# Performance work log

Hardware: AMD Instinct MI355X
Metric: run time of the kernel (lower is better)

Reference implementation:

```python
import jax, jax.numpy as jnp
import numpy as np

HID = 2048 * 3  # infl_ratio = 3
EPS = 1e-5
P_DROP = 0.5


def sign_ste(x):
    # straight-through binarization: sign in fwd, identity in bwd
    return x + jax.lax.stop_gradient(jnp.sign(x) - x)


def batchnorm(x, g, b):
    # training-mode BatchNorm1d: batch stats, biased variance
    m = jnp.mean(x, axis=0)
    v = jnp.mean((x - m) ** 2, axis=0)
    return g * (x - m) / jnp.sqrt(v + EPS) + b


def hardtanh(x):
    return jnp.clip(x, -1.0, 1.0)


def dropout(x, u):
    # u ~ U[0,1); keep where u >= p, scale by 1/(1-p)
    return jnp.where(u >= P_DROP, x / (1.0 - P_DROP), 0.0)


def setup_inputs() -> dict:
    key = jax.random.key(0)
    ks = jax.random.split(key, 16)
    B = 512
    d = {}
    d['x'] = jax.random.normal(ks[0], (B, 784), dtype=jnp.float32)
    d['drop_mask_bin'] = jax.random.uniform(ks[1], (B, HID), dtype=jnp.float32)
    d['drop_mask_real'] = jax.random.uniform(ks[2], (B, HID), dtype=jnp.float32)
    s1 = 1.0 / np.sqrt(784)
    sh = 1.0 / np.sqrt(HID)
    d['w1'] = jax.random.uniform(ks[3], (HID, 784), jnp.float32, -s1, s1)
    d['b1'] = jax.random.uniform(ks[4], (HID,), jnp.float32, -s1, s1)
    d['w2'] = jax.random.uniform(ks[5], (HID, HID), jnp.float32, -sh, sh)
    d['b2'] = jax.random.uniform(ks[6], (HID,), jnp.float32, -sh, sh)
    d['w3'] = jax.random.uniform(ks[7], (HID, HID), jnp.float32, -sh, sh)
    d['b3'] = jax.random.uniform(ks[8], (HID,), jnp.float32, -sh, sh)
    d['w4'] = jax.random.uniform(ks[9], (10, HID), jnp.float32, -sh, sh)
    d['b4'] = jax.random.uniform(ks[10], (10,), jnp.float32, -sh, sh)
    for i, k in zip((1, 2, 3), (ks[11], ks[12], ks[13])):
        d[f'g{i}'] = jnp.ones((HID,), jnp.float32)
        d[f'be{i}'] = jnp.zeros((HID,), jnp.float32)
    return d


def reference(x, drop_mask_bin, drop_mask_real, w1, b1, w2, b2, w3, b3, w4, b4,
              g1, be1, g2, be2, g3, be3):
    sg = jax.lax.stop_gradient
    # layer 1: input dim 784 -> input NOT binarized; weights binarized
    Bout1 = x @ sign_ste(w1).T + b1
    Rout1 = sg(x @ w1.T + b1)
    Bout1 = hardtanh(batchnorm(Bout1, g1, be1))
    Rout1 = sg(hardtanh(batchnorm(Rout1, g1, be1)))
    # layer 2: binarize activations and weights on binary path
    Bout2 = sign_ste(Bout1) @ sign_ste(w2).T + b2
    Rout2 = sg(Rout1 @ w2.T + b2)
    Bout2 = hardtanh(batchnorm(Bout2, g2, be2))
    Rout2 = sg(hardtanh(batchnorm(Rout2, g2, be2)))
    # layer 3 + dropout
    Bout3 = sign_ste(Bout2) @ sign_ste(w3).T + b3
    Rout3 = sg(Rout2 @ w3.T + b3)
    Bout3 = hardtanh(batchnorm(dropout(Bout3, drop_mask_bin), g3, be3))
    Rout3 = sg(hardtanh(batchnorm(dropout(Rout3, drop_mask_real), g3, be3)))
    # classifier (real-valued Linear)
    out = Bout3 @ w4.T + b4
    logp = jax.nn.log_softmax(out, axis=1)
    return (logp, out, Bout1, Rout1, Bout2, Rout2, Bout3, Rout3)
```

## Files before the change

### kernel.cpp

```cpp
#include <hip/hip_runtime.h>


typedef _Float16 f16x8 __attribute__((ext_vector_type(8)));
typedef _Float16 f16x4 __attribute__((ext_vector_type(4)));
typedef float f32x4 __attribute__((ext_vector_type(4)));
typedef int i32x4 __attribute__((ext_vector_type(4)));

#define MFMA16(a, b, c) __builtin_amdgcn_mfma_f32_16x16x32_f16((a), (b), (c), 0, 0, 0)
#define MFMAI8K64(a, b, c) __builtin_amdgcn_mfma_i32_16x16x64_i8((a), (b), (c), 0, 0, 0)

#define HIDC 6144
#define BATCH 512

#define OFF_XH    0ull
#define OFF_Z1LO  851968ull
#define OFF_SB8   13434880ull
#define OFF_RF    16580608ull
#define OFF_STATS 22872064ull
#define OFF_PPART 23068672ull
#define OFF_ZPB   24641536ull
#define OFF_ZPR   37224448ull
#define OFF_ZPR2  49807360ull
#define OFF_ZPR3  62390272ull
#define OFF_W1V   74973184ull
#define OFF_WV    85196800ull
#define OFF_WS8   160694272ull
#define WS_NEED   198443008ull

#define A8_STRIDE 458752ull

__device__ __forceinline__ void load_lds16(const void* g, char* lds) {
  __builtin_amdgcn_global_load_lds((const __attribute__((address_space(1))) void*)g,
                                   (__attribute__((address_space(3))) void*)lds, 16, 0, 0);
}

__global__ __launch_bounds__(256) void k_prep_xq(const float* __restrict__ x,
                                                 char* __restrict__ a8,
                                                 _Float16* __restrict__ xh) {
  int idx = blockIdx.x * 256 + threadIdx.x;
  if (idx >= 512 * 896) return;
  int row = idx / 896, k = idx - row * 896;
  float v = (k < 784) ? x[(size_t)row * 784 + k] : 0.f;
  int q = (int)lrintf(v * 16777216.0f);
  int d0 = ((q + 128) & 255) - 128; q = (q - d0) >> 8;
  int d1 = ((q + 128) & 255) - 128; q = (q - d1) >> 8;
  int d2 = ((q + 128) & 255) - 128; q = (q - d2) >> 8;
  a8[idx] = (char)d0;
  a8[A8_STRIDE + idx] = (char)d1;
  a8[2 * A8_STRIDE + idx] = (char)d2;
  a8[3 * A8_STRIDE + idx] = (char)q;
  if (k < 832) xh[(size_t)row * 832 + k] = (_Float16)v;
}

__global__ __launch_bounds__(256) void k_prep_w1(const float* __restrict__ w,
                                                 char* __restrict__ s1,
                                                 _Float16* __restrict__ w1v) {
  int idx = blockIdx.x * 256 + threadIdx.x;
  if (idx >= 6144 * 896) return;
  int r = idx / 896, k = idx - r * 896;
  float v = (k < 784) ? w[(size_t)r * 784 + k] : 0.f;
  s1[idx] = v > 0.f ? 1 : (v < 0.f ? -1 : 0);
  if (k < 832) w1v[(size_t)r * 832 + k] = (_Float16)v;
}

__global__ __launch_bounds__(256) void k_conv_w23(const float* __restrict__ w,
                                                  _Float16* __restrict__ wv,
                                                  char* __restrict__ ws8) {
  int idx = blockIdx.x * 256 + threadIdx.x;
  size_t o8 = (size_t)idx * 8;
  const float* s = w + o8;
  float4 v0 = *(const float4*)s;
  float4 v1 = *(const float4*)(s + 4);
  float a[8] = {v0.x, v0.y, v0.z, v0.w, v1.x, v1.y, v1.z, v1.w};
  f16x8 hv;
  unsigned long long sbits = 0;
#pragma unroll
  for (int e = 0; e < 8; ++e) {
    hv[e] = (_Float16)a[e];
    char sg = a[e] > 0.f ? 1 : (a[e] < 0.f ? -1 : 0);
    sbits |= ((unsigned long long)(unsigned char)sg) << (8 * e);
  }
  *(f16x8*)(wv + o8) = hv;
  *(unsigned long long*)(ws8 + o8) = sbits;
}

struct MixJob {
  const void* A;
  const void* B;
  float* C;
  int K;
  int kstart;
  int ksteps;
  int is8;
};
struct Mix6 { MixJob j[6]; };

__global__ __launch_bounds__(256) void k_gemm_mix(Mix6 P) {
  __shared__ __align__(16) char smem[65536];
  MixJob J = P.j[0];
  if (blockIdx.z == 1) J = P.j[1];
  if (blockIdx.z == 2) J = P.j[2];
  if (blockIdx.z == 3) J = P.j[3];
  if (blockIdx.z == 4) J = P.j[4];
  if (blockIdx.z == 5) J = P.j[5];
  const int t = threadIdx.x;
  const int lane = t & 63, wid = t >> 6;
  const int wm = wid >> 1, wn = wid & 1;
  const int bn = blockIdx.x, bm = blockIdx.y;
  const size_t K = (size_t)J.K;
  const int nt = J.ksteps;

  if (J.is8) {
    const char* A = (const char*)J.A;
    const char* B = (const char*)J.B;
    i32x4 acc[4][4];
#pragma unroll
    for (int mf = 0; mf < 4; ++mf)
#pragma unroll
      for (int nf = 0; nf < 4; ++nf) acc[mf][nf] = (i32x4){0, 0, 0, 0};

    auto stage = [&](char* dst, int k0) {
#pragma unroll
      for (int i = 0; i < 4; ++i) {
        int p = i * 256 + t;
        int r = p >> 3, c = p & 7;
        int cs = c ^ (r & 7);
        load_lds16(A + (size_t)(bm * 128 + r) * K + k0 + cs * 16, dst + p * 16);
      }
#pragma unroll
      for (int i = 0; i < 4; ++i) {
        int p = i * 256 + t;
        int r = p >> 3, c = p & 7;
        int cs = c ^ (r & 7);
        load_lds16(B + (size_t)(bn * 128 + r) * K + k0 + cs * 16, dst + 16384 + p * 16);
      }
    };

    stage(smem, J.kstart);
    for (int kt = 0; kt < nt; ++kt) {
      char* cbuf = smem + (kt & 1) * 32768;
      char* nbuf = smem + ((kt + 1) & 1) * 32768;
      if (kt + 1 < nt) {
        stage(nbuf, J.kstart + (kt + 1) * 128);
        asm volatile("s_waitcnt vmcnt(8)" ::: "memory");
      } else {
        asm volatile("s_waitcnt vmcnt(0)" ::: "memory");
      }
      __builtin_amdgcn_s_barrier();
      __builtin_amdgcn_s_setprio(1);
#pragma unroll
      for (int kk = 0; kk < 2; ++kk) {
        i32x4 av[4], bv[4];
#pragma unroll
        for (int mf = 0; mf < 4; ++mf) {
          int r = wm * 64 + mf * 16 + (lane & 15);
          int bo = (r * 128 + kk * 64 + (lane >> 4) * 16) ^ ((r & 7) << 4);
          av[mf] = *(const i32x4*)(cbuf + bo);
        }
#pragma unroll
        for (int nf = 0; nf < 4; ++nf) {
          int r = wn * 64 + nf * 16 + (lane & 15);
          int bo = (r * 128 + kk * 64 + (lane >> 4) * 16) ^ ((r & 7) << 4);
          bv[nf] = *(const i32x4*)(cbuf + 16384 + bo);
        }
#pragma unroll
        for (int mf = 0; mf < 4; ++mf)
#pragma unroll
          for (int nf = 0; nf < 4; ++nf) acc[mf][nf] = MFMAI8K64(av[mf], bv[nf], acc[mf][nf]);
      }
      __builtin_amdgcn_s_setprio(0);
      __builtin_amdgcn_s_barrier();
    }
#pragma unroll
    for (int mf = 0; mf < 4; ++mf)
#pragma unroll
      for (int nf = 0; nf < 4; ++nf) {
        int col = bn * 128 + wn * 64 + nf * 16 + (lane & 15);
        int row0 = bm * 128 + wm * 64 + mf * 16 + ((lane >> 4) << 2);
#pragma unroll
        for (int rr = 0; rr < 4; ++rr) {
          J.C[(size_t)(row0 + rr) * HIDC + col] = (float)acc[mf][nf][rr];
        }
      }
  } else {
    const _Float16* A = (const _Float16*)J.A;
    const _Float16* B = (const _Float16*)J.B;
    f32x4 acc[4][4];
#pragma unroll
    for (int mf = 0; mf < 4; ++mf)
#pragma unroll
      for (int nf = 0; nf < 4; ++nf) acc[mf][nf] = (f32x4){0.f, 0.f, 0.f, 0.f};

    auto stage = [&](char* dst, int k0) {
#pragma unroll
      for (int i = 0; i < 4; ++i) {
        int p = i * 256 + t;
        int r = p >> 3, c = p & 7;
        int cs = c ^ (r & 7);
        load_lds16(A + (size_t)(bm * 128 + r) * K + k0 + cs * 8, dst + p * 16);
      }
#pragma unroll
      for (int i = 0; i < 4; ++i) {
        int p = i * 256 + t;
        int r = p >> 3, c = p & 7;
        int cs = c ^ (r & 7);
        load_lds16(B + (size_t)(bn * 128 + r) * K + k0 + cs * 8, dst + 16384 + p * 16);
      }
    };

    stage(smem, J.kstart);
    for (int kt = 0; kt < nt; ++kt) {
      char* cbuf = smem + (kt & 1) * 32768;
      char* nbuf = smem + ((kt + 1) & 1) * 32768;
      if (kt + 1 < nt) {
        stage(nbuf, J.kstart + (kt + 1) * 64);
        asm volatile("s_waitcnt vmcnt(8)" ::: "memory");
      } else {
        asm volatile("s_waitcnt vmcnt(0)" ::: "memory");
      }
      __builtin_amdgcn_s_barrier();
      __builtin_amdgcn_s_setprio(1);
#pragma unroll
      for (int kk = 0; kk < 2; ++kk) {
        f16x8 av[4], bv[4];
#pragma unroll
        for (int mf = 0; mf < 4; ++mf) {
          int r = wm * 64 + mf * 16 + (lane & 15);
          int bo = (r * 128 + kk * 64 + (lane >> 4) * 16) ^ ((r & 7) << 4);
          av[mf] = *(const f16x8*)(cbuf + bo);
        }
#pragma unroll
        for (int nf = 0; nf < 4; ++nf) {
          int r = wn * 64 + nf * 16 + (lane & 15);
          int bo = (r * 128 + kk * 64 + (lane >> 4) * 16) ^ ((r & 7) << 4);
          bv[nf] = *(const f16x8*)(cbuf + 16384 + bo);
        }
#pragma unroll
        for (int mf = 0; mf < 4; ++mf)
#pragma unroll
          for (int nf = 0; nf < 4; ++nf) acc[mf][nf] = MFMA16(av[mf], bv[nf], acc[mf][nf]);
      }
      __builtin_amdgcn_s_setprio(0);
      __builtin_amdgcn_s_barrier();
    }
#pragma unroll
    for (int mf = 0; mf < 4; ++mf)
#pragma unroll
      for (int nf = 0; nf < 4; ++nf) {
        int col = bn * 128 + wn * 64 + nf * 16 + (lane & 15);
        int row0 = bm * 128 + wm * 64 + mf * 16 + ((lane >> 4) << 2);
#pragma unroll
        for (int rr = 0; rr < 4; ++rr) {
          J.C[(size_t)(row0 + rr) * HIDC + col] = acc[mf][nf][rr];
        }
      }
  }
}

__global__ __launch_bounds__(256) void k_combine1(const float* __restrict__ D0,
                                                  const float* __restrict__ D1,
                                                  const float* __restrict__ D2,
                                                  const float* __restrict__ D3,
                                                  float* __restrict__ Zhi,
                                                  float* __restrict__ Zlo) {
  size_t i4 = ((size_t)blockIdx.x * 256 + threadIdx.x) * 4;
  float4 v0 = *(const float4*)(D0 + i4);
  float4 v1 = *(const float4*)(D1 + i4);
  float4 v2 = *(const float4*)(D2 + i4);
  float4 v3 = *(const float4*)(D3 + i4);
  const float* p0 = &v0.x;
  const float* p1 = &v1.x;
  const float* p2 = &v2.x;
  const float* p3 = &v3.x;
  float4 hi, lo;
  float* hp = &hi.x;
  float* lp = &lo.x;
#pragma unroll
  for (int e = 0; e < 4; ++e) {
    double zv = (((double)p3[e] * 256.0 + (double)p2[e]) * 256.0 + (double)p1[e]) * 256.0 +
                (double)p0[e];
    zv *= (1.0 / 16777216.0);
    float h = (float)zv;
    hp[e] = h;
    lp[e] = (float)(zv - (double)h);
  }
  *(float4*)(Zhi + i4) = hi;
  *(float4*)(Zlo + i4) = lo;
}

struct StJob { const float* Z; const float* Zp0; const float* Zp1; const float* Zp2;
               const float* msk; };
struct St2 { StJob j[2]; const float* bias; int dodrop; double* ppart; };

__global__ __launch_bounds__(256) void k_stats_part(St2 P) {
  __shared__ double sm[4][64];
  __shared__ double sq[4][64];
  const int z = blockIdx.z;
  StJob J = z ? P.j[1] : P.j[0];
  const int li = threadIdx.x & 63, rg = threadIdx.x >> 6;
  const int col = blockIdx.x * 64 + li;
  const double bb = P.dodrop ? (double)P.bias[col] : 0.0;
  double s = 0.0, s2 = 0.0;
#pragma unroll 4
  for (int rr = 0; rr < 16; ++rr) {
    int r = blockIdx.y * 64 + rg * 16 + rr;
    size_t i = (size_t)r * HIDC + col;
    double v = (double)J.Z[i];
    if (J.Zp0) v += (double)J.Zp0[i];
    if (J.Zp1) v += (double)J.Zp1[i];
    if (J.Zp2) v += (double)J.Zp2[i];
    if (P.dodrop) v = (J.msk[i] >= 0.5f) ? 2.0 * (v + bb) : 0.0;
    s += v;
    s2 += v * v;
  }
  sm[rg][li] = s;
  sq[rg][li] = s2;
  __syncthreads();
  if (rg == 0) {
    double S = sm[0][li] + sm[1][li] + sm[2][li] + sm[3][li];
    double S2 = sq[0][li] + sq[1][li] + sq[2][li] + sq[3][li];
    size_t o = ((size_t)(z * 8 + blockIdx.y) * 2) * HIDC + col;
    P.ppart[o] = S;
    P.ppart[o + HIDC] = S2;
  }
}

__global__ __launch_bounds__(256) void k_stats_fin(const double* __restrict__ ppart,
                                                   double* __restrict__ stats) {
  const int z = blockIdx.z;
  const int c = blockIdx.x * 256 + threadIdx.x;
  double S = 0.0, S2 = 0.0;
#pragma unroll
  for (int y = 0; y < 8; ++y) {
    size_t o = ((size_t)(z * 8 + y) * 2) * HIDC + c;
    S += ppart[o];
    S2 += ppart[o + HIDC];
  }
  double m = S / 512.0;
  double var = S2 / 512.0 - m * m;
  stats[z * 2 * HIDC + c] = m;
  stats[z * 2 * HIDC + HIDC + c] = 1.0 / sqrt(var + 1e-5);
}

struct BnJob { float* Z; const float* Zp0; const float* Zp1; const float* Zp2;
               void* aux; const float* msk; int auxmode; };
struct Bn2 {
  BnJob j[2];
  const double* stats;
  const float* g; const float* be; const float* bias;
  int dodrop;
};

__global__ __launch_bounds__(256) void k_bn2(Bn2 P) {
  const int z = blockIdx.z;
  BnJob J = z ? P.j[1] : P.j[0];
  const double* m_arr = P.stats + (size_t)z * 2 * HIDC;
  const double* r_arr = m_arr + HIDC;
  int idx = blockIdx.x * 256 + threadIdx.x;
  int row = idx / 1536;
  int c4 = (idx - row * 1536) * 4;
  size_t base = (size_t)row * HIDC + c4;
  float4 zv = *(const float4*)(J.Z + base);
  float zz[4] = {zv.x, zv.y, zv.z, zv.w};
  double ex[4] = {0.0, 0.0, 0.0, 0.0};
  if (J.Zp0) {
    float4 t4 = *(const float4*)(J.Zp0 + base);
    ex[0] += t4.x; ex[1] += t4.y; ex[2] += t4.z; ex[3] += t4.w;
  }
  if (J.Zp1) {
    float4 t4 = *(const float4*)(J.Zp1 + base);
    ex[0] += t4.x; ex[1] += t4.y; ex[2] += t4.z; ex[3] += t4.w;
  }
  if (J.Zp2) {
    float4 t4 = *(const float4*)(J.Zp2 + base);
    ex[0] += t4.x; ex[1] += t4.y; ex[2] += t4.z; ex[3] += t4.w;
  }
  float mk[4] = {1.f, 1.f, 1.f, 1.f};
  if (P.dodrop) {
    float4 t4 = *(const float4*)(J.msk + base);
    mk[0] = t4.x; mk[1] = t4.y; mk[2] = t4.z; mk[3] = t4.w;
  }
  float o[4];
  f16x4 a4;
  int sbits = 0;
#pragma unroll
  for (int e = 0; e < 4; ++e) {
    int c = c4 + e;
    double v = (double)zz[e] + ex[e];
    if (P.dodrop) v = (mk[e] >= 0.5f) ? 2.0 * (v + (double)P.bias[c]) : 0.0;
    double bnv = (double)P.g[c] * ((v - m_arr[c]) * r_arr[c]) + (double)P.be[c];
    bnv = bnv > 1.0 ? 1.0 : (bnv < -1.0 ? -1.0 : bnv);
    o[e] = (float)bnv;
    char sg = bnv > 0.0 ? 1 : (bnv < 0.0 ? -1 : 0);
    sbits |= ((int)(unsigned char)sg) << (8 * e);
    a4[e] = (_Float16)o[e];
  }
  float4 ov = {o[0], o[1], o[2], o[3]};
  *(float4*)(J.Z + base) = ov;
  if (J.auxmode == 0) *(int*)((char*)J.aux + base) = sbits;
  if (J.auxmode == 1) *(f16x4*)((_Float16*)J.aux + base) = a4;
}

__global__ __launch_bounds__(256) void k_head(const float* __restrict__ B3,
                                              const float* __restrict__ w4,
                                              const float* __restrict__ b4,
                                              float* __restrict__ out,
                                              float* __restrict__ logp) {
  const int row = blockIdx.x, t = threadIdx.x;
  float acc[10];
#pragma unroll
  for (int j = 0; j < 10; ++j) acc[j] = 0.f;
  const float* a = B3 + (size_t)row * HIDC;
  for (int k4 = t; k4 < 1536; k4 += 256) {
    float4 av = *(const float4*)(a + k4 * 4);
#pragma unroll
    for (int j = 0; j < 10; ++j) {
      float4 wv = *(const float4*)(w4 + (size_t)j * HIDC + k4 * 4);
      acc[j] += av.x * wv.x + av.y * wv.y + av.z * wv.z + av.w * wv.w;
    }
  }
#pragma unroll
  for (int j = 0; j < 10; ++j)
    for (int off = 32; off; off >>= 1) acc[j] += __shfl_down(acc[j], off);
  __shared__ float sred[4][10];
  int wid = t >> 6, ln = t & 63;
  if (ln == 0)
#pragma unroll
    for (int j = 0; j < 10; ++j) sred[wid][j] = acc[j];
  __syncthreads();
  if (t == 0) {
    double o[10];
    double mx = -1e300;
#pragma unroll
    for (int j = 0; j < 10; ++j) {
      o[j] = (double)sred[0][j] + sred[1][j] + sred[2][j] + sred[3][j] + (double)b4[j];
      mx = o[j] > mx ? o[j] : mx;
    }
    double s = 0.0;
#pragma unroll
    for (int j = 0; j < 10; ++j) s += exp(o[j] - mx);
    double l = log(s) + mx;
#pragma unroll
    for (int j = 0; j < 10; ++j) {
      out[row * 10 + j] = (float)o[j];
      logp[row * 10 + j] = (float)(o[j] - l);
    }
  }
}

extern "C" void kernel_launch(void* const* d_in, const int* in_sizes, int n_in,
                              void* d_out, int out_size, void* d_ws, size_t ws_size,
                              hipStream_t stream) {
  const float* x   = (const float*)d_in[0];
  const float* mkb = (const float*)d_in[1];
  const float* mkr = (const float*)d_in[2];
  const float* w1  = (const float*)d_in[3];
  const float* w2  = (const float*)d_in[5];
  const float* w3  = (const float*)d_in[7];
  const float* b3  = (const float*)d_in[8];
  const float* w4  = (const float*)d_in[9];
  const float* b4  = (const float*)d_in[10];
  const float* g1  = (const float*)d_in[11]; const float* be1 = (const float*)d_in[12];
  const float* g2  = (const float*)d_in[13]; const float* be2 = (const float*)d_in[14];
  const float* g3  = (const float*)d_in[15]; const float* be3 = (const float*)d_in[16];

  float* outp = (float*)d_out;
  float* logp = outp;
  float* outo = outp + 5120;
  float* B1 = outp + 10240;
  float* R1 = outp + 3155968;
  float* B2 = outp + 6301696;
  float* R2 = outp + 9447424;
  float* B3 = outp + 12593152;
  float* R3 = outp + 15738880;

  char* ws = (char*)d_ws;
  _Float16* xh  = (_Float16*)(ws + OFF_XH);
  float* z1lo   = (float*)(ws + OFF_Z1LO);
  char* sB8     = (char*)(ws + OFF_SB8);
  _Float16* rF  = (_Float16*)(ws + OFF_RF);
  double* stats = (double*)(ws + OFF_STATS);
  double* ppart = (double*)(ws + OFF_PPART);
  float* zpb    = (float*)(ws + OFF_ZPB);
  float* zpr    = (float*)(ws + OFF_ZPR);
  float* zpr2   = (float*)(ws + OFF_ZPR2);
  float* zpr3   = (float*)(ws + OFF_ZPR3);
  _Float16* w1v = (_Float16*)(ws + OFF_W1V);
  _Float16* wv  = (_Float16*)(ws + OFF_WV);
  char* ws8     = (char*)(ws + OFF_WS8);
  char* a8 = (char*)(ws + OFF_WS8);
  char* s1 = (char*)(ws + OFF_WS8 + 4ull * A8_STRIDE);

  k_prep_xq<<<1792, 256, 0, stream>>>(x, a8, xh);
  k_prep_w1<<<21504, 256, 0, stream>>>(w1, s1, w1v);
  {
    Mix6 P{};
    P.j[0] = {a8,                 s1, zpb,  896, 0, 7, 1};
    P.j[1] = {a8 + A8_STRIDE,     s1, zpr,  896, 0, 7, 1};
    P.j[2] = {a8 + 2 * A8_STRIDE, s1, zpr2, 896, 0, 7, 1};
    P.j[3] = {a8 + 3 * A8_STRIDE, s1, zpr3, 896, 0, 7, 1};
    P.j[4] = {xh, w1v, R1, 832, 0, 13, 0};
    P.j[5] = P.j[4];
    k_gemm_mix<<<dim3(48, 4, 5), 256, 0, stream>>>(P);
  }
  k_combine1<<<3072, 256, 0, stream>>>(zpb, zpr, zpr2, zpr3, B1, z1lo);
  {
    St2 S{};
    S.j[0] = {B1, z1lo, nullptr, nullptr, nullptr};
    S.j[1] = {R1, nullptr, nullptr, nullptr, nullptr};
    S.bias = nullptr; S.dodrop = 0; S.ppart = ppart;
    k_stats_part<<<dim3(96, 8, 2), 256, 0, stream>>>(S);
    k_stats_fin<<<dim3(24, 1, 2), 256, 0, stream>>>(ppart, stats);
    Bn2 B{};
    B.j[0] = {B1, z1lo, nullptr, nullptr, sB8, nullptr, 0};
    B.j[1] = {R1, nullptr, nullptr, nullptr, rF, nullptr, 1};
    B.stats = stats; B.g = g1; B.be = be1; B.bias = nullptr; B.dodrop = 0;
    k_bn2<<<dim3(3072, 1, 2), 256, 0, stream>>>(B);
  }
  k_conv_w23<<<18432, 256, 0, stream>>>(w2, wv, ws8);
  {
    Mix6 P{};
    P.j[0] = {sB8, ws8, B2,   HIDC, 0,    24, 1};
    P.j[1] = {sB8, ws8, zpb,  HIDC, 3072, 24, 1};
    P.j[2] = {rF,  wv,  R2,   HIDC, 0,    24, 0};
    P.j[3] = {rF,  wv,  zpr,  HIDC, 1536, 24, 0};
    P.j[4] = {rF,  wv,  zpr2, HIDC, 3072, 24, 0};
    P.j[5] = {rF,  wv,  zpr3, HIDC, 4608, 24, 0};
    k_gemm_mix<<<dim3(48, 4, 6), 256, 0, stream>>>(P);
  }
  {
    St2 S{};
    S.j[0] = {B2, zpb, nullptr, nullptr, nullptr};
    S.j[1] = {R2, zpr, zpr2, zpr3, nullptr};
    S.bias = nullptr; S.dodrop = 0; S.ppart = ppart;
    k_stats_part<<<dim3(96, 8, 2), 256, 0, stream>>>(S);
    k_stats_fin<<<dim3(24, 1, 2), 256, 0, stream>>>(ppart, stats);
    Bn2 B{};
    B.j[0] = {B2, zpb, nullptr, nullptr, sB8, nullptr, 0};
    B.j[1] = {R2, zpr, zpr2, zpr3, rF, nullptr, 1};
    B.stats = stats; B.g = g2; B.be = be2; B.bias = nullptr; B.dodrop = 0;
    k_bn2<<<dim3(3072, 1, 2), 256, 0, stream>>>(B);
  }
  k_conv_w23<<<18432, 256, 0, stream>>>(w3, wv, ws8);
  {
    Mix6 P{};
    P.j[0] = {sB8, ws8, B3,   HIDC, 0,    24, 1};
    P.j[1] = {sB8, ws8, zpb,  HIDC, 3072, 24, 1};
    P.j[2] = {rF,  wv,  R3,   HIDC, 0,    24, 0};
    P.j[3] = {rF,  wv,  zpr,  HIDC, 1536, 24, 0};
    P.j[4] = {rF,  wv,  zpr2, HIDC, 3072, 24, 0};
    P.j[5] = {rF,  wv,  zpr3, HIDC, 4608, 24, 0};
    k_gemm_mix<<<dim3(48, 4, 6), 256, 0, stream>>>(P);
  }
  {
    St2 S{};
    S.j[0] = {B3, zpb, nullptr, nullptr, mkb};
    S.j[1] = {R3, zpr, zpr2, zpr3, mkr};
    S.bias = b3; S.dodrop = 1; S.ppart = ppart;
    k_stats_part<<<dim3(96, 8, 2), 256, 0, stream>>>(S);
    k_stats_fin<<<dim3(24, 1, 2), 256, 0, stream>>>(ppart, stats);
    Bn2 B{};
    B.j[0] = {B3, zpb, nullptr, nullptr, nullptr, mkb, 2};
    B.j[1] = {R3, zpr, zpr2, zpr3, nullptr, mkr, 2};
    B.stats = stats; B.g = g3; B.be = be3; B.bias = b3; B.dodrop = 1;
    k_bn2<<<dim3(3072, 1, 2), 256, 0, stream>>>(B);
  }
  k_head<<<512, 256, 0, stream>>>(B3, w4, b4, outo, logp);
}
```

Before: 485.3 us.

## Fold layer-1 digit combine into stats/BN and halve real-path K splits

Removes the separate k_combine1 kernel. The stats and BN kernels now rebuild the layer-1 binary-path result directly from its four base-256 digit partials in double precision, which saves writing and rereading the hi/lo buffers. Layers 2 and 3 now split the real-path GEMM over K into two chunks of 48 instead of four of 24. That cuts the partial buffers the stats and BN passes must read, but each GEMM block does a longer serial K loop and the grid has fewer blocks. Precision changes slightly because only two fp32 partials are summed.

```diff
diff --git a/kernel.cpp b/kernel.cpp
--- a/kernel.cpp
+++ b/kernel.cpp
@@ -257,39 +257,8 @@
   }
 }
 
-__global__ __launch_bounds__(256) void k_combine1(const float* __restrict__ D0,
-                                                  const float* __restrict__ D1,
-                                                  const float* __restrict__ D2,
-                                                  const float* __restrict__ D3,
-                                                  float* __restrict__ Zhi,
-                                                  float* __restrict__ Zlo) {
-  size_t i4 = ((size_t)blockIdx.x * 256 + threadIdx.x) * 4;
-  float4 v0 = *(const float4*)(D0 + i4);
-  float4 v1 = *(const float4*)(D1 + i4);
-  float4 v2 = *(const float4*)(D2 + i4);
-  float4 v3 = *(const float4*)(D3 + i4);
-  const float* p0 = &v0.x;
-  const float* p1 = &v1.x;
-  const float* p2 = &v2.x;
-  const float* p3 = &v3.x;
-  float4 hi, lo;
-  float* hp = &hi.x;
-  float* lp = &lo.x;
-#pragma unroll
-  for (int e = 0; e < 4; ++e) {
-    double zv = (((double)p3[e] * 256.0 + (double)p2[e]) * 256.0 + (double)p1[e]) * 256.0 +
-                (double)p0[e];
-    zv *= (1.0 / 16777216.0);
-    float h = (float)zv;
-    hp[e] = h;
-    lp[e] = (float)(zv - (double)h);
-  }
-  *(float4*)(Zhi + i4) = hi;
-  *(float4*)(Zlo + i4) = lo;
-}
-
 struct StJob { const float* Z; const float* Zp0; const float* Zp1; const float* Zp2;
-               const float* msk; };
+               const float* msk; int digitmode; };
 struct St2 { StJob j[2]; const float* bias; int dodrop; double* ppart; };
 
 __global__ __launch_bounds__(256) void k_stats_part(St2 P) {
@@ -305,10 +274,17 @@
   for (int rr = 0; rr < 16; ++rr) {
     int r = blockIdx.y * 64 + rg * 16 + rr;
     size_t i = (size_t)r * HIDC + col;
-    double v = (double)J.Z[i];
-    if (J.Zp0) v += (double)J.Zp0[i];
-    if (J.Zp1) v += (double)J.Zp1[i];
-    if (J.Zp2) v += (double)J.Zp2[i];
+    double v;
+    if (J.digitmode) {
+      double d0 = (double)J.Z[i], d1 = (double)J.Zp0[i];
+      double d2 = (double)J.Zp1[i], d3 = (double)J.Zp2[i];
+      v = (((d3 * 256.0 + d2) * 256.0 + d1) * 256.0 + d0) * (1.0 / 16777216.0);
+    } else {
+      v = (double)J.Z[i];
+      if (J.Zp0) v += (double)J.Zp0[i];
+      if (J.Zp1) v += (double)J.Zp1[i];
+      if (J.Zp2) v += (double)J.Zp2[i];
+    }
     if (P.dodrop) v = (J.msk[i] >= 0.5f) ? 2.0 * (v + bb) : 0.0;
     s += v;
     s2 += v * v;
@@ -343,7 +319,7 @@
 }
 
 struct BnJob { float* Z; const float* Zp0; const float* Zp1; const float* Zp2;
-               void* aux; const float* msk; int auxmode; };
+               const float* Zp3; void* aux; const float* msk; int auxmode; int digitmode; };
 struct Bn2 {
   BnJob j[2];
   const double* stats;
@@ -360,20 +336,35 @@
   int row = idx / 1536;
   int c4 = (idx - row * 1536) * 4;
   size_t base = (size_t)row * HIDC + c4;
-  float4 zv = *(const float4*)(J.Z + base);
-  float zz[4] = {zv.x, zv.y, zv.z, zv.w};
-  double ex[4] = {0.0, 0.0, 0.0, 0.0};
-  if (J.Zp0) {
-    float4 t4 = *(const float4*)(J.Zp0 + base);
-    ex[0] += t4.x; ex[1] += t4.y; ex[2] += t4.z; ex[3] += t4.w;
-  }
-  if (J.Zp1) {
-    float4 t4 = *(const float4*)(J.Zp1 + base);
-    ex[0] += t4.x; ex[1] += t4.y; ex[2] += t4.z; ex[3] += t4.w;
-  }
-  if (J.Zp2) {
-    float4 t4 = *(const float4*)(J.Zp2 + base);
-    ex[0] += t4.x; ex[1] += t4.y; ex[2] += t4.z; ex[3] += t4.w;
+  double vv[4];
+  if (J.digitmode) {
+    float4 d0 = *(const float4*)(J.Zp0 + base);
+    float4 d1 = *(const float4*)(J.Zp1 + base);
+    float4 d2 = *(const float4*)(J.Zp2 + base);
+    float4 d3 = *(const float4*)(J.Zp3 + base);
+    const float* p0 = &d0.x;
+    const float* p1 = &d1.x;
+    const float* p2 = &d2.x;
+    const float* p3 = &d3.x;
+#pragma unroll
+    for (int e = 0; e < 4; ++e)
+      vv[e] = ((((double)p3[e] * 256.0 + (double)p2[e]) * 256.0 + (double)p1[e]) * 256.0 +
+               (double)p0[e]) * (1.0 / 16777216.0);
+  } else {
+    float4 zv = *(const float4*)(J.Z + base);
+    vv[0] = zv.x; vv[1] = zv.y; vv[2] = zv.z; vv[3] = zv.w;
+    if (J.Zp0) {
+      float4 t4 = *(const float4*)(J.Zp0 + base);
+      vv[0] += t4.x; vv[1] += t4.y; vv[2] += t4.z; vv[3] += t4.w;
+    }
+    if (J.Zp1) {
+      float4 t4 = *(const float4*)(J.Zp1 + base);
+      vv[0] += t4.x; vv[1] += t4.y; vv[2] += t4.z; vv[3] += t4.w;
+    }
+    if (J.Zp2) {
+      float4 t4 = *(const float4*)(J.Zp2 + base);
+      vv[0] += t4.x; vv[1] += t4.y; vv[2] += t4.z; vv[3] += t4.w;
+    }
   }
   float mk[4] = {1.f, 1.f, 1.f, 1.f};
   if (P.dodrop) {
@@ -386,7 +377,7 @@
 #pragma unroll
   for (int e = 0; e < 4; ++e) {
     int c = c4 + e;
-    double v = (double)zz[e] + ex[e];
+    double v = vv[e];
     if (P.dodrop) v = (mk[e] >= 0.5f) ? 2.0 * (v + (double)P.bias[c]) : 0.0;
     double bnv = (double)P.g[c] * ((v - m_arr[c]) * r_arr[c]) + (double)P.be[c];
     bnv = bnv > 1.0 ? 1.0 : (bnv < -1.0 ? -1.0 : bnv);
@@ -476,7 +467,6 @@
 
   char* ws = (char*)d_ws;
   _Float16* xh  = (_Float16*)(ws + OFF_XH);
-  float* z1lo   = (float*)(ws + OFF_Z1LO);
   char* sB8     = (char*)(ws + OFF_SB8);
   _Float16* rF  = (_Float16*)(ws + OFF_RF);
   double* stats = (double*)(ws + OFF_STATS);
@@ -503,65 +493,60 @@
     P.j[5] = P.j[4];
     k_gemm_mix<<<dim3(48, 4, 5), 256, 0, stream>>>(P);
   }
-  k_combine1<<<3072, 256, 0, stream>>>(zpb, zpr, zpr2, zpr3, B1, z1lo);
   {
     St2 S{};
-    S.j[0] = {B1, z1lo, nullptr, nullptr, nullptr};
-    S.j[1] = {R1, nullptr, nullptr, nullptr, nullptr};
+    S.j[0] = {zpb, zpr, zpr2, zpr3, nullptr, 1};
+    S.j[1] = {R1, nullptr, nullptr, nullptr, nullptr, 0};
     S.bias = nullptr; S.dodrop = 0; S.ppart = ppart;
     k_stats_part<<<dim3(96, 8, 2), 256, 0, stream>>>(S);
     k_stats_fin<<<dim3(24, 1, 2), 256, 0, stream>>>(ppart, stats);
     Bn2 B{};
-    B.j[0] = {B1, z1lo, nullptr, nullptr, sB8, nullptr, 0};
-    B.j[1] = {R1, nullptr, nullptr, nullptr, rF, nullptr, 1};
+    B.j[0] = {B1, zpb, zpr, zpr2, zpr3, sB8, nullptr, 0, 1};
+    B.j[1] = {R1, nullptr, nullptr, nullptr, nullptr, rF, nullptr, 1, 0};
     B.stats = stats; B.g = g1; B.be = be1; B.bias = nullptr; B.dodrop = 0;
     k_bn2<<<dim3(3072, 1, 2), 256, 0, stream>>>(B);
   }
   k_conv_w23<<<18432, 256, 0, stream>>>(w2, wv, ws8);
   {
     Mix6 P{};
-    P.j[0] = {sB8, ws8, B2,   HIDC, 0,    24, 1};
-    P.j[1] = {sB8, ws8, zpb,  HIDC, 3072, 24, 1};
-    P.j[2] = {rF,  wv,  R2,   HIDC, 0,    24, 0};
-    P.j[3] = {rF,  wv,  zpr,  HIDC, 1536, 24, 0};
-    P.j[4] = {rF,  wv,  zpr2, HIDC, 3072, 24, 0};
-    P.j[5] = {rF,  wv,  zpr3, HIDC, 4608, 24, 0};
-    k_gemm_mix<<<dim3(48, 4, 6), 256, 0, stream>>>(P);
+    P.j[0] = {sB8, ws8, B2,  HIDC, 0,    24, 1};
+    P.j[1] = {sB8, ws8, zpb, HIDC, 3072, 24, 1};
+    P.j[2] = {rF,  wv,  R2,  HIDC, 0,    48, 0};
+    P.j[3] = {rF,  wv,  zpr, HIDC, 3072, 48, 0};
+    k_gemm_mix<<<dim3(48, 4, 4), 256, 0, stream>>>(P);
   }
   {
     St2 S{};
-    S.j[0] = {B2, zpb, nullptr, nullptr, nullptr};
-    S.j[1] = {R2, zpr, zpr2, zpr3, nullptr};
+    S.j[0] = {B2, zpb, nullptr, nullptr, nullptr, 0};
+    S.j[1] = {R2, zpr, nullptr, nullptr, nullptr, 0};
     S.bias = nullptr; S.dodrop = 0; S.ppart = ppart;
     k_stats_part<<<dim3(96, 8, 2), 256, 0, stream>>>(S);
     k_stats_fin<<<dim3(24, 1, 2), 256, 0, stream>>>(ppart, stats);
     Bn2 B{};
-    B.j[0] = {B2, zpb, nullptr, nullptr, sB8, nullptr, 0};
-    B.j[1] = {R2, zpr, zpr2, zpr3, rF, nullptr, 1};
+    B.j[0] = {B2, zpb, nullptr, nullptr, nullptr, sB8, nullptr, 0, 0};
+    B.j[1] = {R2, zpr, nullptr, nullptr, nullptr, rF, nullptr, 1, 0};
     B.stats = stats; B.g = g2; B.be = be2; B.bias = nullptr; B.dodrop = 0;
     k_bn2<<<dim3(3072, 1, 2), 256, 0, stream>>>(B);
   }
   k_conv_w23<<<18432, 256, 0, stream>>>(w3, wv, ws8);
   {
     Mix6 P{};
-    P.j[0] = {sB8, ws8, B3,   HIDC, 0,    24, 1};
-    P.j[1] = {sB8, ws8, zpb,  HIDC, 3072, 24, 1};
-    P.j[2] = {rF,  wv,  R3,   HIDC, 0,    24, 0};
-    P.j[3] = {rF,  wv,  zpr,  HIDC, 1536, 24, 0};
-    P.j[4] = {rF,  wv,  zpr2, HIDC, 3072, 24, 0};
-    P.j[5] = {rF,  wv,  zpr3, HIDC, 4608, 24, 0};
-    k_gemm_mix<<<dim3(48, 4, 6), 256, 0, stream>>>(P);
+    P.j[0] = {sB8, ws8, B3,  HIDC, 0,    24, 1};
+    P.j[1] = {sB8, ws8, zpb, HIDC, 3072, 24, 1};
+    P.j[2] = {rF,  wv,  R3,  HIDC, 0,    48, 0};
+    P.j[3] = {rF,  wv,  zpr, HIDC, 3072, 48, 0};
+    k_gemm_mix<<<dim3(48, 4, 4), 256, 0, stream>>>(P);
   }
   {
     St2 S{};
-    S.j[0] = {B3, zpb, nullptr, nullptr, mkb};
-    S.j[1] = {R3, zpr, zpr2, zpr3, mkr};
+    S.j[0] = {B3, zpb, nullptr, nullptr, mkb, 0};
+    S.j[1] = {R3, zpr, nullptr, nullptr, mkr, 0};
     S.bias = b3; S.dodrop = 1; S.ppart = ppart;
     k_stats_part<<<dim3(96, 8, 2), 256, 0, stream>>>(S);
     k_stats_fin<<<dim3(24, 1, 2), 256, 0, stream>>>(ppart, stats);
     Bn2 B{};
-    B.j[0] = {B3, zpb, nullptr, nullptr, nullptr, mkb, 2};
-    B.j[1] = {R3, zpr, zpr2, zpr3, nullptr, mkr, 2};
+    B.j[0] = {B3, zpb, nullptr, nullptr, nullptr, nullptr, mkb, 2, 0};
+    B.j[1] = {R3, zpr, nullptr, nullptr, nullptr, nullptr, mkr, 2, 0};
     B.stats = stats; B.g = g3; B.be = be3; B.bias = b3; B.dodrop = 1;
     k_bn2<<<dim3(3072, 1, 2), 256, 0, stream>>>(B);
   }
```

Result: faster. 460.4 us (-5.1%).
